# Kernel optimization log

Measured on AMD Instinct MI355X. Metric: run time of the kernel, lower is better.

## Reference

```python
import jax, jax.numpy as jnp
import numpy as np

NUM_PRICAPS, DIM_PRICAPS = 1152, 8
NUM_OBJCAPS, DIM_OBJCAPS = 10, 16
ROUTINGS = 3


def squash(v, axis=-1):
    norm = jnp.linalg.norm(v, axis=axis, keepdims=True)
    scale = norm ** 2 / (1.0 + norm ** 2) / (norm + 1e-8)
    return scale * v


def conv2d(x, w, b, stride):
    out = jax.lax.conv_general_dilated(
        x, w, window_strides=(stride, stride), padding='VALID',
        dimension_numbers=('NCHW', 'OIHW', 'NCHW'))
    return out + b[None, :, None, None]


def setup_inputs() -> dict:
    key = jax.random.key(0)
    ks = jax.random.split(key, 12)
    f32 = jnp.float32
    x = jax.random.uniform(ks[0], (512, 1, 28, 28), dtype=f32)
    conv1_w = jax.random.normal(ks[1], (256, 1, 9, 9), f32) / np.sqrt(1 * 81)
    conv1_b = jnp.zeros((256,), f32)
    conv2_w = jax.random.normal(ks[2], (256, 256, 9, 9), f32) / np.sqrt(256 * 81)
    conv2_b = jnp.zeros((256,), f32)
    route_w = 0.1 * jax.random.normal(ks[3], (NUM_OBJCAPS, NUM_PRICAPS, DIM_OBJCAPS, DIM_PRICAPS), f32)
    d_in = NUM_OBJCAPS * DIM_OBJCAPS  # 160
    dec1_w = jax.random.normal(ks[4], (512, d_in), f32) / np.sqrt(d_in)
    dec1_b = jnp.zeros((512,), f32)
    dec2_w = jax.random.normal(ks[5], (1024, 512), f32) / np.sqrt(512)
    dec2_b = jnp.zeros((1024,), f32)
    dec3_w = jax.random.normal(ks[6], (784, 1024), f32) / np.sqrt(1024)
    dec3_b = jnp.zeros((784,), f32)
    return {'x': x, 'conv1_w': conv1_w, 'conv1_b': conv1_b,
            'conv2_w': conv2_w, 'conv2_b': conv2_b, 'route_w': route_w,
            'dec1_w': dec1_w, 'dec1_b': dec1_b, 'dec2_w': dec2_w,
            'dec2_b': dec2_b, 'dec3_w': dec3_w, 'dec3_b': dec3_b}


def reference(x, conv1_w, conv1_b, conv2_w, conv2_b, route_w,
              dec1_w, dec1_b, dec2_w, dec2_b, dec3_w, dec3_b):
    B = x.shape[0]
    # Encoder: two convs (no activation in original), then capsulate + squash
    h = conv2d(x, conv1_w, conv1_b, 1)            # [B,256,20,20]
    h = conv2d(h, conv2_w, conv2_b, 2)            # [B,256,6,6]
    pricaps = squash(jnp.transpose(h, (0, 2, 3, 1)).reshape(B, NUM_PRICAPS, DIM_PRICAPS))
    # Votes: weight [o,i,k,d] @ incaps [b,i,d] -> [b,o,i,k]
    hat = jnp.einsum('oikd,bid->boik', route_w, pricaps)  # [B,10,1152,16]
    hat_det = jax.lax.stop_gradient(hat)
    b_log = jnp.zeros((B, NUM_OBJCAPS, NUM_PRICAPS), x.dtype)
    c = jax.nn.softmax(jnp.ones((B, NUM_OBJCAPS, NUM_PRICAPS), x.dtype), axis=1)
    outcaps = None
    for i in range(ROUTINGS):
        if i < ROUTINGS - 1:
            outcaps = squash(jnp.sum(c[:, :, :, None] * hat_det, axis=2, keepdims=True))  # [B,10,1,16]
            b_log = b_log + jnp.sum(outcaps * hat_det, axis=-1)
            c = jax.nn.softmax(b_log, axis=1)
        else:
            outcaps = squash(jnp.sum(c[:, :, :, None] * hat, axis=2, keepdims=True))
    objcaps = outcaps[:, :, 0, :]                 # [B,10,16]
    objcaps_len = jnp.linalg.norm(objcaps, axis=-1)  # [B,10]
    # Decoder: reconstruct only the max-length class capsule
    idx_max = jnp.argmax(objcaps_len, axis=1)
    y_onehot = jax.nn.one_hot(idx_max, NUM_OBJCAPS, dtype=objcaps.dtype)
    oc = (objcaps * y_onehot[:, :, None]).reshape(B, -1)  # [B,160]
    d = jax.nn.relu(oc @ dec1_w.T + dec1_b)
    d = jax.nn.relu(d @ dec2_w.T + dec2_b)
    d = jax.nn.sigmoid(d @ dec3_w.T + dec3_b)
    x_recon = jnp.clip(d.reshape(B, 1, 28, 28), 0.0, 1.0)
    return (objcaps_len, x_recon)
```

## Files before the change

kernel.cpp:

```cpp
#include <hip/hip_runtime.h>

typedef short short8 __attribute__((ext_vector_type(8)));
typedef float floatx4 __attribute__((ext_vector_type(4)));

__device__ __forceinline__ unsigned short bf16rn(float x) {
  union { float f; unsigned int u; } v; v.f = x;
  unsigned int r = v.u + 0x7fffu + ((v.u >> 16) & 1u);
  return (unsigned short)(r >> 16);
}
__device__ __forceinline__ float bf16f(unsigned short h) {
  union { unsigned int u; float f; } v; v.u = ((unsigned int)h) << 16;
  return v.f;
}
__device__ __forceinline__ void gload16(const void* g, void* l) {
  __builtin_amdgcn_global_load_lds((const __attribute__((address_space(1))) unsigned int*)g,
                                   (__attribute__((address_space(3))) unsigned int*)l, 16, 0, 0);
}
__device__ __forceinline__ unsigned swz128(int row) {
  return ((row & 1) << 6) | ((row & 2) << 4) | ((row & 4) << 2);
}

__global__ __launch_bounds__(256) void k_w2p(const float* __restrict__ w2,
                                             unsigned short* __restrict__ w2p) {
  __shared__ float sm[20736];
  const int t = threadIdx.x;
  const int co = blockIdx.x;
  for (int q = t; q < 20736; q += 256) sm[q] = w2[(size_t)co * 20736 + q];
  __syncthreads();
  const unsigned s4 = ((co & 1) << 2) | (co & 2) | ((co & 4) >> 2);
  unsigned short* base = w2p + (size_t)co * 64;
  for (int q = t; q < 5184; q += 256) {
    int kk = q >> 6, r = q & 63, cb = r >> 3, cp = r & 7;
    unsigned src = (unsigned)cp ^ s4;
    int half = src >> 2, oct = src & 3;
    const float* col = &sm[(cb * 32 + oct * 8) * 81 + kk];
    union { unsigned short u[8]; uint4 v; } pk;
#pragma unroll
    for (int j = 0; j < 8; ++j) {
      float v = col[j * 81];
      unsigned short hi = bf16rn(v);
      pk.u[j] = half ? bf16rn(v - bf16f(hi)) : hi;
    }
    *(uint4*)(base + (size_t)(kk * 8 + cb) * 16384 + cp * 8) = pk.v;
  }
}

__global__ __launch_bounds__(256) void k_conv1(const float* __restrict__ x, const float* __restrict__ w1,
                                               const float* __restrict__ b1,
                                               unsigned short* __restrict__ h1h,
                                               unsigned short* __restrict__ h1l, int b0) {
  __shared__ float xs[784];
  __shared__ float wsm[64 * 81];
  const int t = threadIdx.x;
  const int b = b0 + blockIdx.x;
  const int coq = blockIdx.y;
  for (int q = t; q < 784; q += 256) xs[q] = x[(size_t)b * 784 + q];
  for (int q = t; q < 5184; q += 256) wsm[q] = w1[coq * 5184 + q];
  __syncthreads();
  const int col = t & 63, yg = t >> 6;
  const int co = coq * 64 + col;
  const float bv = b1[co];
  unsigned short* oh = h1h + (size_t)blockIdx.x * 102400 + co;
  unsigned short* ol = h1l + (size_t)blockIdx.x * 102400 + co;
  for (int yy = 0; yy < 5; ++yy) {
    const int y = yg * 5 + yy;
    float acc[20];
#pragma unroll
    for (int i = 0; i < 20; ++i) acc[i] = bv;
    for (int ky = 0; ky < 9; ++ky) {
      float row[28];
#pragma unroll
      for (int cc = 0; cc < 28; ++cc) row[cc] = xs[(y + ky) * 28 + cc];
#pragma unroll
      for (int kx = 0; kx < 9; ++kx) {
        float wv = wsm[col * 81 + ky * 9 + kx];
#pragma unroll
        for (int xx = 0; xx < 20; ++xx) acc[xx] += row[xx + kx] * wv;
      }
    }
#pragma unroll
    for (int xx = 0; xx < 20; ++xx) {
      unsigned short hi = bf16rn(acc[xx]);
      unsigned short lo = bf16rn(acc[xx] - bf16f(hi));
      size_t p = (size_t)(y * 20 + xx) * 256;
      oh[p] = hi; ol[p] = lo;
    }
  }
}

__global__ __launch_bounds__(256) void k_conv2m(const unsigned short* __restrict__ h1h,
                                                const unsigned short* __restrict__ h1l,
                                                const unsigned short* __restrict__ w2p,
                                                float* __restrict__ part, int b0) {
  __shared__ __align__(16) char smem[40960];
  const int t = threadIdx.x;
  const int lin = blockIdx.x + 144 * blockIdx.z;
  const int xcd = lin & 7, idx = lin >> 3;
  const int zz = xcd & 3;
  const int n0 = ((xcd >> 2) * 72 + idx) * 64;
  const int kk0 = (zz == 0) ? 0 : (21 + 20 * (zz - 1));
  const int kkn = (zz == 0) ? 21 : 20;

  const int wid = t >> 6, lane = t & 63;
  const int l15 = lane & 15, l4 = lane >> 4;
  const int brow = t >> 2, bc4 = t & 3;
  size_t bsrc;
  {
    int nloc = n0 + brow;
    int bi = nloc / 36, pp = nloc - bi * 36;
    int oy = pp / 6, ox = pp - oy * 6;
    bsrc = ((size_t)((bi * 20 + 2 * oy) * 20 + 2 * ox)) * 256;
  }
  const unsigned bswz = swz128(brow);
  const unsigned bo_hi = (unsigned)(brow * 128) + (((unsigned)(bc4 * 16)) ^ bswz);
  const unsigned bo_lo = (unsigned)(brow * 128) + (((unsigned)(64 + bc4 * 16)) ^ bswz);

  floatx4 acc[4][4];
#pragma unroll
  for (int i = 0; i < 4; ++i)
#pragma unroll
    for (int j = 0; j < 4; ++j) acc[i][j] = (floatx4)0.f;

  for (int kq = 0; kq < kkn; ++kq) {
    const int kk = kk0 + kq;
    const int ky = kk / 9, kx = kk - ky * 9;
    const int koff = (ky * 20 + kx) * 256;
    for (int cb = 0; cb < 8; ++cb) {
      const unsigned short* abase = w2p + (size_t)(kk * 8 + cb) * 16384;
#pragma unroll
      for (int j = 0; j < 8; ++j) {
        const int seg = j * 4 + wid;
        gload16(abase + seg * 512 + lane * 8, smem + seg * 1024);
      }
      {
        const unsigned short* sh = h1h + bsrc + koff + cb * 32 + bc4 * 8;
        const unsigned short* sl = h1l + bsrc + koff + cb * 32 + bc4 * 8;
        uint4 vh = *(const uint4*)sh;
        uint4 vl = *(const uint4*)sl;
        *(uint4*)(smem + 32768 + bo_hi) = vh;
        *(uint4*)(smem + 32768 + bo_lo) = vl;
      }
      __syncthreads();
      short8 bh[4], blo[4];
#pragma unroll
      for (int nf = 0; nf < 4; ++nf) {
        const int br = nf * 16 + l15;
        const unsigned s = swz128(br);
        bh[nf] = *(const short8*)(smem + 32768 + br * 128 + (((unsigned)(l4 * 16)) ^ s));
        blo[nf] = *(const short8*)(smem + 32768 + br * 128 + (((unsigned)(64 + l4 * 16)) ^ s));
      }
#pragma unroll
      for (int mf = 0; mf < 4; ++mf) {
        const int ar = wid * 64 + mf * 16 + l15;
        const unsigned s = swz128(ar);
        short8 ah = *(const short8*)(smem + ar * 128 + (((unsigned)(l4 * 16)) ^ s));
        short8 al = *(const short8*)(smem + ar * 128 + (((unsigned)(64 + l4 * 16)) ^ s));
#pragma unroll
        for (int nf = 0; nf < 4; ++nf) {
          acc[mf][nf] = __builtin_amdgcn_mfma_f32_16x16x32_bf16(ah, bh[nf], acc[mf][nf], 0, 0, 0);
          acc[mf][nf] = __builtin_amdgcn_mfma_f32_16x16x32_bf16(ah, blo[nf], acc[mf][nf], 0, 0, 0);
          acc[mf][nf] = __builtin_amdgcn_mfma_f32_16x16x32_bf16(al, bh[nf], acc[mf][nf], 0, 0, 0);
        }
      }
      __syncthreads();
    }
  }
  float* po = part + (size_t)zz * 4718592;
#pragma unroll
  for (int mf = 0; mf < 4; ++mf) {
#pragma unroll
    for (int nf = 0; nf < 4; ++nf) {
      int cog = wid * 64 + mf * 16 + l4 * 4;
      int ng = b0 * 36 + n0 + nf * 16 + l15;
      *(floatx4*)&po[(size_t)ng * 256 + cog] = acc[mf][nf];
    }
  }
}

__global__ __launch_bounds__(256) void k_redsquash(const float* __restrict__ part,
                                                   const float* __restrict__ b2,
                                                   float* __restrict__ pri) {
  const int idx = blockIdx.x * 256 + threadIdx.x;
  const int n = idx >> 5, cap = idx & 31;
  const size_t o = (size_t)n * 256 + cap * 8;
  float s[8];
#pragma unroll
  for (int j = 0; j < 8; ++j) s[j] = b2[cap * 8 + j];
#pragma unroll
  for (int z = 0; z < 4; ++z) {
    const float4 a0 = *(const float4*)&part[(size_t)z * 4718592 + o];
    const float4 a1 = *(const float4*)&part[(size_t)z * 4718592 + o + 4];
    s[0] += a0.x; s[1] += a0.y; s[2] += a0.z; s[3] += a0.w;
    s[4] += a1.x; s[5] += a1.y; s[6] += a1.z; s[7] += a1.w;
  }
  float ss = 0.f;
#pragma unroll
  for (int j = 0; j < 8; ++j) ss += s[j] * s[j];
  float nn = sqrtf(ss);
  float sc = ss / (1.f + ss) / (nn + 1e-8f);
  float4 o0, o1;
  o0.x = s[0] * sc; o0.y = s[1] * sc; o0.z = s[2] * sc; o0.w = s[3] * sc;
  o1.x = s[4] * sc; o1.y = s[5] * sc; o1.z = s[6] * sc; o1.w = s[7] * sc;
  *(float4*)&pri[o] = o0;
  *(float4*)&pri[o + 4] = o1;
}

__global__ __launch_bounds__(256, 2) void k_passA(const float* __restrict__ rw, const float* __restrict__ pri,
                                                  const float* __restrict__ cbuf, float* __restrict__ spart,
                                                  int iter) {
  __shared__ __align__(16) float rw_s[16 * 516];
  __shared__ __align__(16) float p_s[16 * 516];
  __shared__ float c_s[1024];
  const int t = threadIdx.x;
  const int b0 = blockIdx.x * 16, i0 = blockIdx.y * 64, o = blockIdx.z;
  const float* rsrc = rw + (size_t)o * 147456 + (size_t)i0 * 128;
  for (int q = t; q < 8192; q += 256) {
    int il = q >> 7, rem = q & 127;
    rw_s[(rem >> 3) * 516 + il * 8 + (rem & 7)] = rsrc[q];
  }
  for (int q = t; q < 8192; q += 256) {
    int bl = q >> 9, off = q & 511;
    p_s[bl * 516 + off] = pri[(size_t)(b0 + bl) * 9216 + i0 * 8 + off];
  }
  if (iter > 0) {
    for (int q = t; q < 1024; q += 256) {
      int bl = q >> 6, il = q & 63;
      c_s[q] = cbuf[(size_t)((b0 + bl) * 10 + o) * 1152 + i0 + il];
    }
  }
  __syncthreads();
  const int d = t & 15, bl = t >> 4;
  float acc = 0.f;
  for (int il = 0; il < 64; ++il) {
    float cv = (iter == 0) ? 0.1f : c_s[bl * 64 + il];
    float4 p0 = *(float4*)&p_s[bl * 516 + il * 8];
    float4 p1 = *(float4*)&p_s[bl * 516 + il * 8 + 4];
    float4 r0 = *(float4*)&rw_s[d * 516 + il * 8];
    float4 r1 = *(float4*)&rw_s[d * 516 + il * 8 + 4];
    float dt = r0.x * p0.x + r0.y * p0.y + r0.z * p0.z + r0.w * p0.w +
               r1.x * p1.x + r1.y * p1.y + r1.z * p1.z + r1.w * p1.w;
    acc += cv * dt;
  }
  spart[((size_t)blockIdx.y * 512 + (b0 + bl)) * 160 + o * 16 + d] = acc;
}

__global__ __launch_bounds__(256) void k_reduce(const float* __restrict__ spart, float* __restrict__ outc,
                                                float* __restrict__ len_out, int final_) {
  const int t = threadIdx.x;
  const int b = blockIdx.x;
  if (t >= 160) return;
  const int o = t / 16, d = t & 15;
  float s = 0.f;
  for (int ic = 0; ic < 18; ++ic) s += spart[((size_t)ic * 512 + b) * 160 + t];
  float ss = s * s;
  ss += __shfl_xor(ss, 1, 16);
  ss += __shfl_xor(ss, 2, 16);
  ss += __shfl_xor(ss, 4, 16);
  ss += __shfl_xor(ss, 8, 16);
  float n = sqrtf(ss);
  float sc = ss / (1.f + ss) / (n + 1e-8f);
  outc[(size_t)b * 160 + t] = sc * s;
  if (final_ && d == 0) len_out[b * 10 + o] = sc * n;
}

__global__ __launch_bounds__(256, 2) void k_passB(const float* __restrict__ rw, const float* __restrict__ pri,
                                                  const float* __restrict__ outc, float* __restrict__ blog,
                                                  int accum) {
  __shared__ __align__(16) float rw_s[16 * 516];
  __shared__ __align__(16) float p_s[16 * 516];
  __shared__ float oc_s[256];
  const int t = threadIdx.x;
  const int b0 = blockIdx.x * 16, i0 = blockIdx.y * 64, o = blockIdx.z;
  const float* rsrc = rw + (size_t)o * 147456 + (size_t)i0 * 128;
  for (int q = t; q < 8192; q += 256) {
    int il = q >> 7, rem = q & 127;
    rw_s[(rem >> 3) * 516 + il * 8 + (rem & 7)] = rsrc[q];
  }
  for (int q = t; q < 8192; q += 256) {
    int bl = q >> 9, off = q & 511;
    p_s[bl * 516 + off] = pri[(size_t)(b0 + bl) * 9216 + i0 * 8 + off];
  }
  oc_s[t] = outc[(size_t)(b0 + (t >> 4)) * 160 + o * 16 + (t & 15)];
  __syncthreads();
  const int il0 = t & 15, bl = t >> 4;
  float ocv[16];
#pragma unroll
  for (int k = 0; k < 16; ++k) ocv[k] = oc_s[bl * 16 + k];
#pragma unroll
  for (int is = 0; is < 4; ++is) {
    const int il = is * 16 + il0;
    float4 p0 = *(float4*)&p_s[bl * 516 + il * 8];
    float4 p1 = *(float4*)&p_s[bl * 516 + il * 8 + 4];
    float acc = 0.f;
#pragma unroll
    for (int dd = 0; dd < 16; ++dd) {
      float4 r0 = *(float4*)&rw_s[dd * 516 + il * 8];
      float4 r1 = *(float4*)&rw_s[dd * 516 + il * 8 + 4];
      float h = r0.x * p0.x + r0.y * p0.y + r0.z * p0.z + r0.w * p0.w +
                r1.x * p1.x + r1.y * p1.y + r1.z * p1.z + r1.w * p1.w;
      acc += h * ocv[dd];
    }
    size_t gi = (size_t)((b0 + bl) * 10 + o) * 1152 + i0 + il;
    blog[gi] = accum ? (blog[gi] + acc) : acc;
  }
}

__global__ __launch_bounds__(256) void k_softmax(const float* __restrict__ blog, float* __restrict__ cbuf) {
  const int b = blockIdx.x;
  const int i = blockIdx.y * 256 + threadIdx.x;
  if (i >= 1152) return;
  float v[10];
  float m = -1e30f;
#pragma unroll
  for (int o = 0; o < 10; ++o) {
    v[o] = blog[(size_t)(b * 10 + o) * 1152 + i];
    m = fmaxf(m, v[o]);
  }
  float s = 0.f;
#pragma unroll
  for (int o = 0; o < 10; ++o) {
    v[o] = __expf(v[o] - m);
    s += v[o];
  }
  float inv = 1.f / s;
#pragma unroll
  for (int o = 0; o < 10; ++o) cbuf[(size_t)(b * 10 + o) * 1152 + i] = v[o] * inv;
}

__global__ __launch_bounds__(256) void k_argmax(const float* __restrict__ len_, const float* __restrict__ outc,
                                                int* __restrict__ win, float* __restrict__ oc16) {
  const int b = blockIdx.x * 256 + threadIdx.x;
  if (b >= 512) return;
  float best = len_[b * 10];
  int wi = 0;
  for (int o = 1; o < 10; ++o) {
    float v = len_[b * 10 + o];
    if (v > best) { best = v; wi = o; }
  }
  win[b] = wi;
  for (int k = 0; k < 16; ++k) oc16[b * 16 + k] = outc[(size_t)b * 160 + wi * 16 + k];
}

__global__ __launch_bounds__(256) void k_dec1(const float* __restrict__ oc16, const int* __restrict__ win,
                                              const float* __restrict__ w, const float* __restrict__ bias,
                                              float* __restrict__ d1) {
  const int b = blockIdx.x, t = threadIdx.x;
  const int wi = win[b];
  float ocv[16];
#pragma unroll
  for (int k = 0; k < 16; ++k) ocv[k] = oc16[b * 16 + k];
#pragma unroll
  for (int rep = 0; rep < 2; ++rep) {
    int j = t + rep * 256;
    const float* wr = w + (size_t)j * 160 + wi * 16;
    float acc = bias[j];
#pragma unroll
    for (int k = 0; k < 16; ++k) acc += ocv[k] * wr[k];
    d1[(size_t)b * 512 + j] = fmaxf(acc, 0.f);
  }
}

template <int K, int ACT>
__global__ __launch_bounds__(256) void k_fc(const float* __restrict__ in, const float* __restrict__ w,
                                            const float* __restrict__ bias, float* __restrict__ out, int M) {
  __shared__ __align__(16) float w_s[16 * 64];
  __shared__ __align__(16) float i_s[16 * 64];
  const int t = threadIdx.x;
  const int j0 = blockIdx.x * 64, b0 = blockIdx.y * 64;
  const int tx = t & 15, ty = t >> 4;
  const int jl = tx * 4, bl = ty * 4;
  float acc[4][4];
#pragma unroll
  for (int i = 0; i < 4; ++i)
#pragma unroll
    for (int j = 0; j < 4; ++j) acc[i][j] = 0.f;
  const int rr = t >> 2, kq = (t & 3) * 4;
  for (int k0 = 0; k0 < K; k0 += 16) {
    __syncthreads();
    float4 wv = make_float4(0.f, 0.f, 0.f, 0.f);
    if (j0 + rr < M) wv = *(const float4*)&w[(size_t)(j0 + rr) * K + k0 + kq];
    float4 iv = *(const float4*)&in[(size_t)(b0 + rr) * K + k0 + kq];
    w_s[(kq + 0) * 64 + rr] = wv.x;
    w_s[(kq + 1) * 64 + rr] = wv.y;
    w_s[(kq + 2) * 64 + rr] = wv.z;
    w_s[(kq + 3) * 64 + rr] = wv.w;
    i_s[(kq + 0) * 64 + rr] = iv.x;
    i_s[(kq + 1) * 64 + rr] = iv.y;
    i_s[(kq + 2) * 64 + rr] = iv.z;
    i_s[(kq + 3) * 64 + rr] = iv.w;
    __syncthreads();
#pragma unroll
    for (int k = 0; k < 16; ++k) {
      float4 a = *(float4*)&w_s[k * 64 + jl];
      float4 v = *(float4*)&i_s[k * 64 + bl];
      float av[4] = {a.x, a.y, a.z, a.w};
      float vv[4] = {v.x, v.y, v.z, v.w};
#pragma unroll
      for (int jj = 0; jj < 4; ++jj)
#pragma unroll
        for (int bb = 0; bb < 4; ++bb) acc[jj][bb] += av[jj] * vv[bb];
    }
  }
#pragma unroll
  for (int jj = 0; jj < 4; ++jj) {
    int j = j0 + jl + jj;
    if (j >= M) continue;
    float bs = bias[j];
#pragma unroll
    for (int bb = 0; bb < 4; ++bb) {
      float v = acc[jj][bb] + bs;
      if (ACT == 0) {
        v = fmaxf(v, 0.f);
      } else {
        v = 1.f / (1.f + __expf(-v));
        v = fminf(fmaxf(v, 0.f), 1.f);
      }
      out[(size_t)(b0 + bl + bb) * M + j] = v;
    }
  }
}

extern "C" void kernel_launch(void* const* d_in, const int* in_sizes, int n_in,
                              void* d_out, int out_size, void* d_ws, size_t ws_size,
                              hipStream_t stream) {
  (void)in_sizes; (void)n_in; (void)out_size; (void)ws_size;
  const float* x   = (const float*)d_in[0];
  const float* w1  = (const float*)d_in[1];
  const float* b1  = (const float*)d_in[2];
  const float* w2  = (const float*)d_in[3];
  const float* b2  = (const float*)d_in[4];
  const float* rw  = (const float*)d_in[5];
  const float* d1w = (const float*)d_in[6];
  const float* d1b = (const float*)d_in[7];
  const float* d2w = (const float*)d_in[8];
  const float* d2b = (const float*)d_in[9];
  const float* d3w = (const float*)d_in[10];
  const float* d3b = (const float*)d_in[11];
  float* out = (float*)d_out;

  char* wsb = (char*)d_ws;
  size_t cur = 0;
  auto alloc = [&](size_t bytes) -> char* {
    char* p = wsb + cur;
    cur += (bytes + 255) & ~(size_t)255;
    return p;
  };
  unsigned short* W2P = (unsigned short*)alloc(21233664);
  float* PART = (float*)alloc(75497472);
  float* PRI  = (float*)alloc(18874368);
  float* OUTC = (float*)alloc(327680);
  float* OC   = (float*)alloc(32768);
  int*   WIN  = (int*)alloc(2048);
  float* D1   = (float*)alloc(1048576);
  float* D2   = (float*)alloc(2097152);
  unsigned short* H1H = (unsigned short*)alloc(52428800);
  unsigned short* H1L = (unsigned short*)alloc(52428800);
  float* C  = (float*)H1H;
  float* BL = (float*)((char*)H1H + 23592960);
  float* SP = (float*)((char*)H1H + 47185920);

  k_w2p<<<256, 256, 0, stream>>>(w2, W2P);
  for (int b0 = 0; b0 < 512; b0 += 256) {
    k_conv1<<<dim3(256, 4), 256, 0, stream>>>(x, w1, b1, H1H, H1L, b0);
    k_conv2m<<<dim3(144, 1, 4), 256, 0, stream>>>(H1H, H1L, W2P, PART, b0);
  }
  k_redsquash<<<2304, 256, 0, stream>>>(PART, b2, PRI);

  dim3 gAB(32, 18, 10);
  k_passA<<<gAB, 256, 0, stream>>>(rw, PRI, C, SP, 0);
  k_reduce<<<512, 256, 0, stream>>>(SP, OUTC, out, 0);
  k_passB<<<gAB, 256, 0, stream>>>(rw, PRI, OUTC, BL, 0);
  k_softmax<<<dim3(512, 5), 256, 0, stream>>>(BL, C);
  k_passA<<<gAB, 256, 0, stream>>>(rw, PRI, C, SP, 1);
  k_reduce<<<512, 256, 0, stream>>>(SP, OUTC, out, 0);
  k_passB<<<gAB, 256, 0, stream>>>(rw, PRI, OUTC, BL, 1);
  k_softmax<<<dim3(512, 5), 256, 0, stream>>>(BL, C);
  k_passA<<<gAB, 256, 0, stream>>>(rw, PRI, C, SP, 2);
  k_reduce<<<512, 256, 0, stream>>>(SP, OUTC, out, 1);

  k_argmax<<<2, 256, 0, stream>>>(out, OUTC, WIN, OC);
  k_dec1<<<512, 256, 0, stream>>>(OC, WIN, d1w, d1b, D1);
  k_fc<512, 0><<<dim3(16, 8), 256, 0, stream>>>(D1, d2w, d2b, D2, 1024);
  k_fc<1024, 1><<<dim3(13, 8), 256, 0, stream>>>(D2, d3w, d3b, out + 5120, 784);
}
```

Before: 1.423 ms.

## Double-buffer conv2 MFMA kernel shared memory to overlap loads with compute

Converts the conv2 GEMM main loop into a software-pipelined, double-buffered loop. The next weight tile (global_load_lds) and activation tile (register prefetch) are issued before computing on the current buffer, and one barrier per step replaces two. This hides global-memory latency behind the MFMA work. It doubles LDS use to 80KB per block, which may lower occupancy.

```diff
diff --git a/kernel.cpp b/kernel.cpp
--- a/kernel.cpp
+++ b/kernel.cpp
@@ -92,7 +92,7 @@
                                                 const unsigned short* __restrict__ h1l,
                                                 const unsigned short* __restrict__ w2p,
                                                 float* __restrict__ part, int b0) {
-  __shared__ __align__(16) char smem[40960];
+  __shared__ __align__(16) char smem[81920];
   const int t = threadIdx.x;
   const int lin = blockIdx.x + 144 * blockIdx.z;
   const int xcd = lin & 7, idx = lin >> 3;
@@ -121,49 +121,72 @@
 #pragma unroll
     for (int j = 0; j < 4; ++j) acc[i][j] = (floatx4)0.f;
 
-  for (int kq = 0; kq < kkn; ++kq) {
-    const int kk = kk0 + kq;
+  const int S = kkn * 8;
+
+  {
+    const int kk = kk0;
     const int ky = kk / 9, kx = kk - ky * 9;
-    const int koff = (ky * 20 + kx) * 256;
-    for (int cb = 0; cb < 8; ++cb) {
+    const int koff = (ky * 20 + kx) * 256 + bc4 * 8;
+    uint4 vh = *(const uint4*)(h1h + bsrc + koff);
+    uint4 vl = *(const uint4*)(h1l + bsrc + koff);
+    const unsigned short* abase = w2p + (size_t)(kk * 8) * 16384;
+#pragma unroll
+    for (int j = 0; j < 8; ++j) {
+      const int seg = j * 4 + wid;
+      gload16(abase + seg * 512 + lane * 8, smem + seg * 1024);
+    }
+    *(uint4*)(smem + 32768 + bo_hi) = vh;
+    *(uint4*)(smem + 32768 + bo_lo) = vl;
+  }
+  __syncthreads();
+
+  unsigned cur = 0;
+  for (int s = 0; s < S; ++s) {
+    char* bcur = smem + cur;
+    char* bnxt = smem + (cur ^ 40960u);
+    const bool pf = (s + 1 < S);
+    uint4 vh, vl;
+    if (pf) {
+      const int s1 = s + 1;
+      const int kk = kk0 + (s1 >> 3), cb = s1 & 7;
+      const int ky = kk / 9, kx = kk - ky * 9;
+      const int koff = (ky * 20 + kx) * 256 + cb * 32 + bc4 * 8;
+      vh = *(const uint4*)(h1h + bsrc + koff);
+      vl = *(const uint4*)(h1l + bsrc + koff);
       const unsigned short* abase = w2p + (size_t)(kk * 8 + cb) * 16384;
 #pragma unroll
       for (int j = 0; j < 8; ++j) {
         const int seg = j * 4 + wid;
-        gload16(abase + seg * 512 + lane * 8, smem + seg * 1024);
+        gload16(abase + seg * 512 + lane * 8, bnxt + seg * 1024);
       }
-      {
-        const unsigned short* sh = h1h + bsrc + koff + cb * 32 + bc4 * 8;
-        const unsigned short* sl = h1l + bsrc + koff + cb * 32 + bc4 * 8;
-        uint4 vh = *(const uint4*)sh;
-        uint4 vl = *(const uint4*)sl;
-        *(uint4*)(smem + 32768 + bo_hi) = vh;
-        *(uint4*)(smem + 32768 + bo_lo) = vl;
+    }
+    short8 bh[4], blo[4];
+#pragma unroll
+    for (int nf = 0; nf < 4; ++nf) {
+      const int br = nf * 16 + l15;
+      const unsigned sw = swz128(br);
+      bh[nf]  = *(const short8*)(bcur + 32768 + br * 128 + (((unsigned)(l4 * 16)) ^ sw));
+      blo[nf] = *(const short8*)(bcur + 32768 + br * 128 + (((unsigned)(64 + l4 * 16)) ^ sw));
+    }
+#pragma unroll
+    for (int mf = 0; mf < 4; ++mf) {
+      const int ar = wid * 64 + mf * 16 + l15;
+      const unsigned sw = swz128(ar);
+      short8 ah = *(const short8*)(bcur + ar * 128 + (((unsigned)(l4 * 16)) ^ sw));
+      short8 al = *(const short8*)(bcur + ar * 128 + (((unsigned)(64 + l4 * 16)) ^ sw));
+#pragma unroll
+      for (int nf = 0; nf < 4; ++nf) {
+        acc[mf][nf] = __builtin_amdgcn_mfma_f32_16x16x32_bf16(ah, bh[nf], acc[mf][nf], 0, 0, 0);
+        acc[mf][nf] = __builtin_amdgcn_mfma_f32_16x16x32_bf16(ah, blo[nf], acc[mf][nf], 0, 0, 0);
+        acc[mf][nf] = __builtin_amdgcn_mfma_f32_16x16x32_bf16(al, bh[nf], acc[mf][nf], 0, 0, 0);
       }
-      __syncthreads();
-      short8 bh[4], blo[4];
-#pragma unroll
-      for (int nf = 0; nf < 4; ++nf) {
-        const int br = nf * 16 + l15;
-        const unsigned s = swz128(br);
-        bh[nf] = *(const short8*)(smem + 32768 + br * 128 + (((unsigned)(l4 * 16)) ^ s));
-        blo[nf] = *(const short8*)(smem + 32768 + br * 128 + (((unsigned)(64 + l4 * 16)) ^ s));
-      }
-#pragma unroll
-      for (int mf = 0; mf < 4; ++mf) {
-        const int ar = wid * 64 + mf * 16 + l15;
-        const unsigned s = swz128(ar);
-        short8 ah = *(const short8*)(smem + ar * 128 + (((unsigned)(l4 * 16)) ^ s));
-        short8 al = *(const short8*)(smem + ar * 128 + (((unsigned)(64 + l4 * 16)) ^ s));
-#pragma unroll
-        for (int nf = 0; nf < 4; ++nf) {
-          acc[mf][nf] = __builtin_amdgcn_mfma_f32_16x16x32_bf16(ah, bh[nf], acc[mf][nf], 0, 0, 0);
-          acc[mf][nf] = __builtin_amdgcn_mfma_f32_16x16x32_bf16(ah, blo[nf], acc[mf][nf], 0, 0, 0);
-          acc[mf][nf] = __builtin_amdgcn_mfma_f32_16x16x32_bf16(al, bh[nf], acc[mf][nf], 0, 0, 0);
-        }
-      }
-      __syncthreads();
-    }
+    }
+    if (pf) {
+      *(uint4*)(bnxt + 32768 + bo_hi) = vh;
+      *(uint4*)(bnxt + 32768 + bo_lo) = vl;
+    }
+    __syncthreads();
+    cur ^= 40960u;
   }
   float* po = part + (size_t)zz * 4718592;
 #pragma unroll
```

Result: slower. 1.598 ms (+12.3%).

## Merge conv2 batch halves into one launch with wider 128-column tiles

Applied to the files above, without the earlier changes.

When the workspace is large enough, conv1 output for all 512 images is kept resident and conv2 runs as a single launch over the full batch. The new kernel uses 256x128 output tiles (8 N-fragments per wave), which doubles the reuse of each loaded weight tile and halves the number of weight loads. Later buffers are overlaid on the H1 region once it is no longer needed. In exchange it needs more accumulator registers per thread (launch bounds of 2 blocks per unit) and about 300MB of workspace; if the workspace is smaller, the old two-launch path runs instead.

```diff
diff --git a/kernel.cpp b/kernel.cpp
--- a/kernel.cpp
+++ b/kernel.cpp
@@ -172,6 +172,103 @@
     for (int nf = 0; nf < 4; ++nf) {
       int cog = wid * 64 + mf * 16 + l4 * 4;
       int ng = b0 * 36 + n0 + nf * 16 + l15;
+      *(floatx4*)&po[(size_t)ng * 256 + cog] = acc[mf][nf];
+    }
+  }
+}
+
+__global__ __launch_bounds__(256, 2) void k_conv2m_big(const unsigned short* __restrict__ h1h,
+                                                       const unsigned short* __restrict__ h1l,
+                                                       const unsigned short* __restrict__ w2p,
+                                                       float* __restrict__ part) {
+  __shared__ __align__(16) char smem[49152];
+  const int t = threadIdx.x;
+  const int lin = blockIdx.x + 144 * blockIdx.z;
+  const int xcd = lin & 7, idx = lin >> 3;
+  const int zz = xcd & 3;
+  const int nb = (xcd >> 2) * 72 + idx;
+  const int n0 = nb * 128;
+  const int kk0 = (zz == 0) ? 0 : (21 + 20 * (zz - 1));
+  const int kkn = (zz == 0) ? 21 : 20;
+
+  const int wid = t >> 6, lane = t & 63;
+  const int l15 = lane & 15, l4 = lane >> 4;
+
+  const int brow = t >> 1, bc2 = t & 1;
+  size_t bsrc;
+  {
+    int nloc = n0 + brow;
+    int bi = nloc / 36, pp = nloc - bi * 36;
+    int oy = pp / 6, ox = pp - oy * 6;
+    bsrc = ((size_t)((bi * 20 + 2 * oy) * 20 + 2 * ox)) * 256;
+  }
+  const unsigned bswz = swz128(brow);
+  const int c0 = bc2 * 2, c1 = bc2 * 2 + 1;
+  const unsigned wo_h0 = (unsigned)(brow * 128) + (((unsigned)(c0 * 16)) ^ bswz);
+  const unsigned wo_h1 = (unsigned)(brow * 128) + (((unsigned)(c1 * 16)) ^ bswz);
+  const unsigned wo_l0 = (unsigned)(brow * 128) + (((unsigned)(64 + c0 * 16)) ^ bswz);
+  const unsigned wo_l1 = (unsigned)(brow * 128) + (((unsigned)(64 + c1 * 16)) ^ bswz);
+
+  floatx4 acc[4][8];
+#pragma unroll
+  for (int i = 0; i < 4; ++i)
+#pragma unroll
+    for (int j = 0; j < 8; ++j) acc[i][j] = (floatx4)0.f;
+
+  for (int kq = 0; kq < kkn; ++kq) {
+    const int kk = kk0 + kq;
+    const int ky = kk / 9, kx = kk - ky * 9;
+    const int koff = (ky * 20 + kx) * 256;
+    for (int cb = 0; cb < 8; ++cb) {
+      const unsigned cbo = (unsigned)(koff + cb * 32);
+      const unsigned short* abase = w2p + (size_t)(kk * 8 + cb) * 16384;
+#pragma unroll
+      for (int j = 0; j < 8; ++j) {
+        const int seg = j * 4 + wid;
+        gload16(abase + seg * 512 + lane * 8, smem + seg * 1024);
+      }
+      {
+        uint4 vh0 = *(const uint4*)(h1h + bsrc + cbo + c0 * 8);
+        uint4 vh1 = *(const uint4*)(h1h + bsrc + cbo + c1 * 8);
+        uint4 vl0 = *(const uint4*)(h1l + bsrc + cbo + c0 * 8);
+        uint4 vl1 = *(const uint4*)(h1l + bsrc + cbo + c1 * 8);
+        *(uint4*)(smem + 32768 + wo_h0) = vh0;
+        *(uint4*)(smem + 32768 + wo_h1) = vh1;
+        *(uint4*)(smem + 32768 + wo_l0) = vl0;
+        *(uint4*)(smem + 32768 + wo_l1) = vl1;
+      }
+      __syncthreads();
+      short8 ah[4], al[4];
+#pragma unroll
+      for (int mf = 0; mf < 4; ++mf) {
+        const int ar = wid * 64 + mf * 16 + l15;
+        const unsigned s = swz128(ar);
+        ah[mf] = *(const short8*)(smem + ar * 128 + (((unsigned)(l4 * 16)) ^ s));
+        al[mf] = *(const short8*)(smem + ar * 128 + (((unsigned)(64 + l4 * 16)) ^ s));
+      }
+#pragma unroll
+      for (int nf = 0; nf < 8; ++nf) {
+        const int br = nf * 16 + l15;
+        const unsigned s = swz128(br);
+        short8 bh  = *(const short8*)(smem + 32768 + br * 128 + (((unsigned)(l4 * 16)) ^ s));
+        short8 blo = *(const short8*)(smem + 32768 + br * 128 + (((unsigned)(64 + l4 * 16)) ^ s));
+#pragma unroll
+        for (int mf = 0; mf < 4; ++mf) {
+          acc[mf][nf] = __builtin_amdgcn_mfma_f32_16x16x32_bf16(ah[mf], bh, acc[mf][nf], 0, 0, 0);
+          acc[mf][nf] = __builtin_amdgcn_mfma_f32_16x16x32_bf16(ah[mf], blo, acc[mf][nf], 0, 0, 0);
+          acc[mf][nf] = __builtin_amdgcn_mfma_f32_16x16x32_bf16(al[mf], bh, acc[mf][nf], 0, 0, 0);
+        }
+      }
+      __syncthreads();
+    }
+  }
+  float* po = part + (size_t)zz * 4718592;
+#pragma unroll
+  for (int mf = 0; mf < 4; ++mf) {
+#pragma unroll
+    for (int nf = 0; nf < 8; ++nf) {
+      int cog = wid * 64 + mf * 16 + l4 * 4;
+      int ng = n0 + nf * 16 + l15;
       *(floatx4*)&po[(size_t)ng * 256 + cog] = acc[mf][nf];
     }
   }
@@ -423,7 +520,7 @@
 extern "C" void kernel_launch(void* const* d_in, const int* in_sizes, int n_in,
                               void* d_out, int out_size, void* d_ws, size_t ws_size,
                               hipStream_t stream) {
-  (void)in_sizes; (void)n_in; (void)out_size; (void)ws_size;
+  (void)in_sizes; (void)n_in; (void)out_size;
   const float* x   = (const float*)d_in[0];
   const float* w1  = (const float*)d_in[1];
   const float* b1  = (const float*)d_in[2];
@@ -445,24 +542,55 @@
     cur += (bytes + 255) & ~(size_t)255;
     return p;
   };
-  unsigned short* W2P = (unsigned short*)alloc(21233664);
-  float* PART = (float*)alloc(75497472);
-  float* PRI  = (float*)alloc(18874368);
-  float* OUTC = (float*)alloc(327680);
-  float* OC   = (float*)alloc(32768);
-  int*   WIN  = (int*)alloc(2048);
-  float* D1   = (float*)alloc(1048576);
-  float* D2   = (float*)alloc(2097152);
-  unsigned short* H1H = (unsigned short*)alloc(52428800);
-  unsigned short* H1L = (unsigned short*)alloc(52428800);
-  float* C  = (float*)H1H;
-  float* BL = (float*)((char*)H1H + 23592960);
-  float* SP = (float*)((char*)H1H + 47185920);
+
+  const bool merged = (ws_size >= (size_t)306446336ULL);
+
+  unsigned short *W2P, *H1H, *H1L;
+  float *PART, *PRI, *OUTC, *OC, *D1, *D2, *C, *BL, *SP;
+  int* WIN;
+
+  if (merged) {
+    W2P  = (unsigned short*)alloc(21233664);
+    PART = (float*)alloc(75497472);
+    H1H  = (unsigned short*)alloc(104857600);
+    H1L  = (unsigned short*)alloc(104857600);
+    char* ov = (char*)H1H;
+    PRI  = (float*)ov;               ov += 18874368;
+    OUTC = (float*)ov;               ov += 327680;
+    OC   = (float*)ov;               ov += 32768;
+    WIN  = (int*)ov;                 ov += 2048;
+    D1   = (float*)ov;               ov += 1048576;
+    D2   = (float*)ov;               ov += 2097152;
+    C    = (float*)ov;               ov += 23592960;
+    BL   = (float*)ov;               ov += 23592960;
+    SP   = (float*)ov;               ov += 5898240;
+  } else {
+    W2P  = (unsigned short*)alloc(21233664);
+    PART = (float*)alloc(75497472);
+    PRI  = (float*)alloc(18874368);
+    OUTC = (float*)alloc(327680);
+    OC   = (float*)alloc(32768);
+    WIN  = (int*)alloc(2048);
+    D1   = (float*)alloc(1048576);
+    D2   = (float*)alloc(2097152);
+    H1H  = (unsigned short*)alloc(52428800);
+    H1L  = (unsigned short*)alloc(52428800);
+    C    = (float*)H1H;
+    BL   = (float*)((char*)H1H + 23592960);
+    SP   = (float*)((char*)H1H + 47185920);
+  }
 
   k_w2p<<<256, 256, 0, stream>>>(w2, W2P);
-  for (int b0 = 0; b0 < 512; b0 += 256) {
-    k_conv1<<<dim3(256, 4), 256, 0, stream>>>(x, w1, b1, H1H, H1L, b0);
-    k_conv2m<<<dim3(144, 1, 4), 256, 0, stream>>>(H1H, H1L, W2P, PART, b0);
+  if (merged) {
+    k_conv1<<<dim3(256, 4), 256, 0, stream>>>(x, w1, b1, H1H, H1L, 0);
+    k_conv1<<<dim3(256, 4), 256, 0, stream>>>(x, w1, b1, H1H + (size_t)256 * 102400,
+                                              H1L + (size_t)256 * 102400, 256);
+    k_conv2m_big<<<dim3(144, 1, 4), 256, 0, stream>>>(H1H, H1L, W2P, PART);
+  } else {
+    for (int b0 = 0; b0 < 512; b0 += 256) {
+      k_conv1<<<dim3(256, 4), 256, 0, stream>>>(x, w1, b1, H1H, H1L, b0);
+      k_conv2m<<<dim3(144, 1, 4), 256, 0, stream>>>(H1H, H1L, W2P, PART, b0);
+    }
   }
   k_redsquash<<<2304, 256, 0, stream>>>(PART, b2, PRI);
 
```

After: 1.414 ms. Within noise of the previous version (-0.7%).

## Widen conv2 GEMM tile to 128 columns with 8-way split-K and per-chunk reduce

Applied to the files above, without the earlier changes.

The conv2 MFMA kernel now computes a 256x128 output tile per block instead of 256x64, doubling the accumulators and reusing each A (weight) fragment across 8 B fragments. To keep the grid size the same, split-K goes from 4 to 8 partitions. The partial-sum reduce and squash now run once per 256-image chunk, so the partial buffer is halved per chunk. This cuts weight traffic into LDS per output, at the cost of higher register pressure (launch bounds 256,2), more partial-sum traffic per output, and one extra reduce launch.

```diff
diff --git a/kernel.cpp b/kernel.cpp
--- a/kernel.cpp
+++ b/kernel.cpp
@@ -88,22 +88,24 @@
   }
 }
 
-__global__ __launch_bounds__(256) void k_conv2m(const unsigned short* __restrict__ h1h,
-                                                const unsigned short* __restrict__ h1l,
-                                                const unsigned short* __restrict__ w2p,
-                                                float* __restrict__ part, int b0) {
-  __shared__ __align__(16) char smem[40960];
+__global__ __launch_bounds__(256, 2) void k_conv2m_big(const unsigned short* __restrict__ h1h,
+                                                       const unsigned short* __restrict__ h1l,
+                                                       const unsigned short* __restrict__ w2p,
+                                                       float* __restrict__ part) {
+  __shared__ __align__(16) char smem[49152];
   const int t = threadIdx.x;
   const int lin = blockIdx.x + 144 * blockIdx.z;
   const int xcd = lin & 7, idx = lin >> 3;
-  const int zz = xcd & 3;
-  const int n0 = ((xcd >> 2) * 72 + idx) * 64;
-  const int kk0 = (zz == 0) ? 0 : (21 + 20 * (zz - 1));
-  const int kkn = (zz == 0) ? 21 : 20;
+  const int half = xcd >> 2, jj = xcd & 3;
+  const int g = jj + 4 * (idx & 1);
+  const int n0 = (half * 36 + (idx >> 1)) * 128;
+  const int kk0 = (g == 0) ? 0 : (11 + 10 * (g - 1));
+  const int kkn = (g == 0) ? 11 : 10;
 
   const int wid = t >> 6, lane = t & 63;
   const int l15 = lane & 15, l4 = lane >> 4;
-  const int brow = t >> 2, bc4 = t & 3;
+
+  const int brow = t >> 1, bc2 = t & 1;
   size_t bsrc;
   {
     int nloc = n0 + brow;
@@ -112,20 +114,24 @@
     bsrc = ((size_t)((bi * 20 + 2 * oy) * 20 + 2 * ox)) * 256;
   }
   const unsigned bswz = swz128(brow);
-  const unsigned bo_hi = (unsigned)(brow * 128) + (((unsigned)(bc4 * 16)) ^ bswz);
-  const unsigned bo_lo = (unsigned)(brow * 128) + (((unsigned)(64 + bc4 * 16)) ^ bswz);
-
-  floatx4 acc[4][4];
+  const int c0 = bc2 * 2, c1 = bc2 * 2 + 1;
+  const unsigned wo_h0 = (unsigned)(brow * 128) + (((unsigned)(c0 * 16)) ^ bswz);
+  const unsigned wo_h1 = (unsigned)(brow * 128) + (((unsigned)(c1 * 16)) ^ bswz);
+  const unsigned wo_l0 = (unsigned)(brow * 128) + (((unsigned)(64 + c0 * 16)) ^ bswz);
+  const unsigned wo_l1 = (unsigned)(brow * 128) + (((unsigned)(64 + c1 * 16)) ^ bswz);
+
+  floatx4 acc[4][8];
 #pragma unroll
   for (int i = 0; i < 4; ++i)
 #pragma unroll
-    for (int j = 0; j < 4; ++j) acc[i][j] = (floatx4)0.f;
+    for (int j = 0; j < 8; ++j) acc[i][j] = (floatx4)0.f;
 
   for (int kq = 0; kq < kkn; ++kq) {
     const int kk = kk0 + kq;
     const int ky = kk / 9, kx = kk - ky * 9;
     const int koff = (ky * 20 + kx) * 256;
     for (int cb = 0; cb < 8; ++cb) {
+      const unsigned cbo = (unsigned)(koff + cb * 32);
       const unsigned short* abase = w2p + (size_t)(kk * 8 + cb) * 16384;
 #pragma unroll
       for (int j = 0; j < 8; ++j) {
@@ -133,45 +139,47 @@
         gload16(abase + seg * 512 + lane * 8, smem + seg * 1024);
       }
       {
-        const unsigned short* sh = h1h + bsrc + koff + cb * 32 + bc4 * 8;
-        const unsigned short* sl = h1l + bsrc + koff + cb * 32 + bc4 * 8;
-        uint4 vh = *(const uint4*)sh;
-        uint4 vl = *(const uint4*)sl;
-        *(uint4*)(smem + 32768 + bo_hi) = vh;
-        *(uint4*)(smem + 32768 + bo_lo) = vl;
+        uint4 vh0 = *(const uint4*)(h1h + bsrc + cbo + c0 * 8);
+        uint4 vh1 = *(const uint4*)(h1h + bsrc + cbo + c1 * 8);
+        uint4 vl0 = *(const uint4*)(h1l + bsrc + cbo + c0 * 8);
+        uint4 vl1 = *(const uint4*)(h1l + bsrc + cbo + c1 * 8);
+        *(uint4*)(smem + 32768 + wo_h0) = vh0;
+        *(uint4*)(smem + 32768 + wo_h1) = vh1;
+        *(uint4*)(smem + 32768 + wo_l0) = vl0;
+        *(uint4*)(smem + 32768 + wo_l1) = vl1;
       }
       __syncthreads();
-      short8 bh[4], blo[4];
-#pragma unroll
-      for (int nf = 0; nf < 4; ++nf) {
-        const int br = nf * 16 + l15;
-        const unsigned s = swz128(br);
-        bh[nf] = *(const short8*)(smem + 32768 + br * 128 + (((unsigned)(l4 * 16)) ^ s));
-        blo[nf] = *(const short8*)(smem + 32768 + br * 128 + (((unsigned)(64 + l4 * 16)) ^ s));
-      }
+      short8 ah[4], al[4];
 #pragma unroll
       for (int mf = 0; mf < 4; ++mf) {
         const int ar = wid * 64 + mf * 16 + l15;
         const unsigned s = swz128(ar);
-        short8 ah = *(const short8*)(smem + ar * 128 + (((unsigned)(l4 * 16)) ^ s));
-        short8 al = *(const short8*)(smem + ar * 128 + (((unsigned)(64 + l4 * 16)) ^ s));
-#pragma unroll
-        for (int nf = 0; nf < 4; ++nf) {
-          acc[mf][nf] = __builtin_amdgcn_mfma_f32_16x16x32_bf16(ah, bh[nf], acc[mf][nf], 0, 0, 0);
-          acc[mf][nf] = __builtin_amdgcn_mfma_f32_16x16x32_bf16(ah, blo[nf], acc[mf][nf], 0, 0, 0);
-          acc[mf][nf] = __builtin_amdgcn_mfma_f32_16x16x32_bf16(al, bh[nf], acc[mf][nf], 0, 0, 0);
+        ah[mf] = *(const short8*)(smem + ar * 128 + (((unsigned)(l4 * 16)) ^ s));
+        al[mf] = *(const short8*)(smem + ar * 128 + (((unsigned)(64 + l4 * 16)) ^ s));
+      }
+#pragma unroll
+      for (int nf = 0; nf < 8; ++nf) {
+        const int br = nf * 16 + l15;
+        const unsigned s = swz128(br);
+        short8 bh  = *(const short8*)(smem + 32768 + br * 128 + (((unsigned)(l4 * 16)) ^ s));
+        short8 blo = *(const short8*)(smem + 32768 + br * 128 + (((unsigned)(64 + l4 * 16)) ^ s));
+#pragma unroll
+        for (int mf = 0; mf < 4; ++mf) {
+          acc[mf][nf] = __builtin_amdgcn_mfma_f32_16x16x32_bf16(ah[mf], bh, acc[mf][nf], 0, 0, 0);
+          acc[mf][nf] = __builtin_amdgcn_mfma_f32_16x16x32_bf16(ah[mf], blo, acc[mf][nf], 0, 0, 0);
+          acc[mf][nf] = __builtin_amdgcn_mfma_f32_16x16x32_bf16(al[mf], bh, acc[mf][nf], 0, 0, 0);
         }
       }
       __syncthreads();
     }
   }
-  float* po = part + (size_t)zz * 4718592;
+  float* po = part + (size_t)g * 2359296;
 #pragma unroll
   for (int mf = 0; mf < 4; ++mf) {
 #pragma unroll
-    for (int nf = 0; nf < 4; ++nf) {
+    for (int nf = 0; nf < 8; ++nf) {
       int cog = wid * 64 + mf * 16 + l4 * 4;
-      int ng = b0 * 36 + n0 + nf * 16 + l15;
+      int ng = n0 + nf * 16 + l15;
       *(floatx4*)&po[(size_t)ng * 256 + cog] = acc[mf][nf];
     }
   }
@@ -187,9 +195,9 @@
 #pragma unroll
   for (int j = 0; j < 8; ++j) s[j] = b2[cap * 8 + j];
 #pragma unroll
-  for (int z = 0; z < 4; ++z) {
-    const float4 a0 = *(const float4*)&part[(size_t)z * 4718592 + o];
-    const float4 a1 = *(const float4*)&part[(size_t)z * 4718592 + o + 4];
+  for (int z = 0; z < 8; ++z) {
+    const float4 a0 = *(const float4*)&part[(size_t)z * 2359296 + o];
+    const float4 a1 = *(const float4*)&part[(size_t)z * 2359296 + o + 4];
     s[0] += a0.x; s[1] += a0.y; s[2] += a0.z; s[3] += a0.w;
     s[4] += a1.x; s[5] += a1.y; s[6] += a1.z; s[7] += a1.w;
   }
@@ -462,9 +470,9 @@
   k_w2p<<<256, 256, 0, stream>>>(w2, W2P);
   for (int b0 = 0; b0 < 512; b0 += 256) {
     k_conv1<<<dim3(256, 4), 256, 0, stream>>>(x, w1, b1, H1H, H1L, b0);
-    k_conv2m<<<dim3(144, 1, 4), 256, 0, stream>>>(H1H, H1L, W2P, PART, b0);
-  }
-  k_redsquash<<<2304, 256, 0, stream>>>(PART, b2, PRI);
+    k_conv2m_big<<<dim3(144, 1, 4), 256, 0, stream>>>(H1H, H1L, W2P, PART);
+    k_redsquash<<<1152, 256, 0, stream>>>(PART, b2, PRI + (size_t)b0 * 36 * 256);
+  }
 
   dim3 gAB(32, 18, 10);
   k_passA<<<gAB, 256, 0, stream>>>(rw, PRI, C, SP, 0);
```

New measurement: 1.476 ms. 1.04x slower.
